# Optimization experiments

Hardware: AMD Instinct MI355X
Metric: run time of the kernel (lower is better)

## Reference

```python
import jax, jax.numpy as jnp
import numpy as np

D_MODEL = 1024
NUM_HEADS = 16
D_K = D_MODEL // NUM_HEADS


def setup_inputs() -> dict:
    key = jax.random.key(0)
    ks = jax.random.split(key, 5)
    sd = np.sqrt(2.0 / (D_MODEL + D_MODEL))
    x = jax.random.normal(ks[0], (2, 2048, D_MODEL), dtype=jnp.float32)
    # weights stored as [out_features, in_features] like torch Linear
    w_q = jax.random.normal(ks[1], (D_MODEL, D_MODEL), dtype=jnp.float32) * (sd * sd)
    w_k = jax.random.normal(ks[2], (D_MODEL, D_MODEL), dtype=jnp.float32) * (sd * sd)
    w_v = jax.random.normal(ks[3], (D_MODEL, D_MODEL), dtype=jnp.float32) * (sd * sd)
    w_o = jax.random.normal(ks[4], (D_MODEL, D_MODEL), dtype=jnp.float32) * (sd * sd)
    return {"x": x, "w_q": w_q, "w_k": w_k, "w_v": w_v, "w_o": w_o}


def reference(x, w_q, w_k, w_v, w_o):
    B, S, D = x.shape
    H, Dk = NUM_HEADS, D_K
    # projections: x @ W.T
    q = (x @ w_q.T).reshape(B, S, H, Dk).transpose(0, 2, 1, 3)  # [B,H,S,Dk]
    k = (x @ w_k.T).reshape(B, S, H, Dk).transpose(0, 2, 1, 3)
    v = (x @ w_v.T).reshape(B, S, H, Dk).transpose(0, 2, 1, 3)
    scale = 1.0 / np.sqrt(Dk).astype(np.float32)
    scores = jnp.einsum('bhqd,bhkd->bhqk', q, k) * scale  # [B,H,S,S]
    causal = jnp.tril(jnp.ones((S, S), dtype=bool))
    scores = jnp.where(causal, scores, -jnp.inf)
    weights = jax.nn.softmax(scores, axis=-1)
    attn = jnp.einsum('bhqk,bhkd->bhqd', weights, v)  # [B,H,S,Dk]
    attn = attn.transpose(0, 2, 1, 3).reshape(B, S, D)
    return attn @ w_o.T
```

## Files before the change

kernel.cpp:

```cpp
#include <hip/hip_runtime.h>

typedef __attribute__((ext_vector_type(8))) short short8;
typedef __attribute__((ext_vector_type(4))) float f32x4;
typedef __attribute__((ext_vector_type(16))) float f32x16;
typedef __attribute__((ext_vector_type(2))) unsigned int u32x2;

#define DM 1024
#define SL 2048
#define NH 16
#define DKH 64
#define NB 2

__device__ __forceinline__ unsigned short f2bf(float f) {
    union { float f; unsigned int u; } a; a.f = f;
    unsigned int r = a.u + 0x7FFFu + ((a.u >> 16) & 1u);
    return (unsigned short)(r >> 16);
}

__device__ __forceinline__ void gl_lds16(const void* g, void* l) {
    __builtin_amdgcn_global_load_lds(
        (__attribute__((address_space(1))) void*)(g),
        (__attribute__((address_space(3))) void*)(l), 16, 0, 0);
}

__device__ __forceinline__ unsigned int cvtpk_bf16(float lo, float hi) {
    unsigned int r;
    asm("v_cvt_pk_bf16_f32 %0, %1, %2" : "=v"(r) : "v"(lo), "v"(hi));
    return r;
}

__device__ __forceinline__ void pl32swap(unsigned int &a, unsigned int &b) {
    u32x2 r = __builtin_amdgcn_permlane32_swap(a, b, false, false);
    a = r[0]; b = r[1];
}
__device__ __forceinline__ void pl32swapf(float &a, float &b) {
    unsigned int ua = __float_as_uint(a), ub = __float_as_uint(b);
    pl32swap(ua, ub);
    a = __uint_as_float(ua); b = __uint_as_float(ub);
}

__global__ __launch_bounds__(256) void convert_kernel(
    const float* __restrict__ x,  const float* __restrict__ wq,
    const float* __restrict__ wk, const float* __restrict__ wv,
    const float* __restrict__ wo,
    unsigned short* __restrict__ xb,  unsigned short* __restrict__ wqb,
    unsigned short* __restrict__ wkb, unsigned short* __restrict__ wvb,
    unsigned short* __restrict__ wob)
{
    const int NX = NB * SL * DM;
    const int NW = DM * DM;
    int t4 = (blockIdx.x * 256 + threadIdx.x) * 4;
    const float* src; unsigned short* dst; int off; float scale = 1.0f;
    if (t4 < NX)              { src = x;  dst = xb;  off = t4; }
    else if (t4 < NX + NW)    { src = wq; dst = wqb; off = t4 - NX; scale = 0.125f * 1.44269504088896f; }
    else if (t4 < NX + 2*NW)  { src = wk; dst = wkb; off = t4 - NX - NW; }
    else if (t4 < NX + 3*NW)  { src = wv; dst = wvb; off = t4 - NX - 2*NW; }
    else                      { src = wo; dst = wob; off = t4 - NX - 3*NW; }
    float4 v = *(const float4*)(src + off);
    unsigned long long p =
        (unsigned long long)f2bf(v.x * scale)
      | ((unsigned long long)f2bf(v.y * scale) << 16)
      | ((unsigned long long)f2bf(v.z * scale) << 32)
      | ((unsigned long long)f2bf(v.w * scale) << 48);
    *(unsigned long long*)(dst + off) = p;
}

template<int MODE>
__global__ __launch_bounds__(256) void gemm_bt(
    const unsigned short* __restrict__ A,
    const unsigned short* __restrict__ Bw,
    unsigned short* __restrict__ oq, unsigned short* __restrict__ ok,
    unsigned short* __restrict__ ov, float* __restrict__ of)
{
    __shared__ __align__(16) unsigned short As[128 * 64];
    __shared__ __align__(16) unsigned short Bs[128 * 64];
    const int tid  = threadIdx.x;
    const int lane = tid & 63;
    const int wave = tid >> 6;
    const int wm = (wave >> 1) * 64, wn = (wave & 1) * 64;
    const int bx = blockIdx.x, by = blockIdx.y;
    const int c    = lane & 15;
    const int kg16 = (lane >> 4) * 16;
    const int swz  = (c & 7) << 4;

    f32x4 acc[4][4];
    #pragma unroll
    for (int i = 0; i < 4; i++)
        #pragma unroll
        for (int j = 0; j < 4; j++) acc[i][j] = (f32x4){0.f, 0.f, 0.f, 0.f};

    const char* Ab = (const char*)A  + by * 128 * (DM * 2);
    const char* Bb = (const char*)Bw + bx * 128 * (DM * 2);

    for (int k0 = 0; k0 < DM; k0 += 64) {
        #pragma unroll
        for (int i = 0; i < 4; i++) {
            int o  = i * 4096 + tid * 16;
            int r  = o >> 7;
            int cb = o & 127;
            int src = r * (DM * 2) + k0 * 2 + (cb ^ ((r & 7) << 4));
            gl_lds16(Ab + src, (char*)As + o);
            gl_lds16(Bb + src, (char*)Bs + o);
        }
        __syncthreads();
        #pragma unroll
        for (int kk = 0; kk < 2; kk++) {
            short8 a[4], bfr[4];
            #pragma unroll
            for (int mi = 0; mi < 4; mi++)
                a[mi] = *(const short8*)((const char*)As
                        + (wm + mi * 16 + c) * 128 + ((kk * 64 + kg16) ^ swz));
            #pragma unroll
            for (int ni = 0; ni < 4; ni++)
                bfr[ni] = *(const short8*)((const char*)Bs
                        + (wn + ni * 16 + c) * 128 + ((kk * 64 + kg16) ^ swz));
            #pragma unroll
            for (int mi = 0; mi < 4; mi++)
                #pragma unroll
                for (int ni = 0; ni < 4; ni++)
                    acc[mi][ni] = __builtin_amdgcn_mfma_f32_16x16x32_bf16(
                        a[mi], bfr[ni], acc[mi][ni], 0, 0, 0);
        }
        __syncthreads();
    }

    const int r4 = (lane >> 4) * 4;
    if (MODE == 0) {
        const int mat = (bx * 128) >> 10;
        unsigned short* outb = (mat == 0) ? oq : (mat == 1) ? ok : ov;
        const int nb = bx * 128 - (mat << 10);
        #pragma unroll
        for (int mi = 0; mi < 4; mi++) {
            int m_g = by * 128 + wm + mi * 16 + r4;
            int b_  = m_g >> 11, s_ = m_g & 2047;
            #pragma unroll
            for (int ni = 0; ni < 4; ni++) {
                int n_l = nb + wn + ni * 16 + c;
                int h = n_l >> 6, dk = n_l & 63;
                #pragma unroll
                for (int j = 0; j < 4; j++)
                    outb[((b_ * NH + h) * SL + (s_ + j)) * DKH + dk] = f2bf(acc[mi][ni][j]);
            }
        }
    } else {
        #pragma unroll
        for (int mi = 0; mi < 4; mi++) {
            int m_g = by * 128 + wm + mi * 16 + r4;
            #pragma unroll
            for (int ni = 0; ni < 4; ni++) {
                int n_g = bx * 128 + wn + ni * 16 + c;
                #pragma unroll
                for (int j = 0; j < 4; j++)
                    of[(m_g + j) * DM + n_g] = acc[mi][ni][j];
            }
        }
    }
}

__global__ __launch_bounds__(128) void attn_kernel(
    const unsigned short* __restrict__ Q,
    const unsigned short* __restrict__ K,
    const unsigned short* __restrict__ V,
    unsigned short* __restrict__ O,
    unsigned short* __restrict__ partO,
    float* __restrict__ ml)
{
    __shared__ __align__(16) unsigned short Kl[2][64 * 64];
    __shared__ __align__(16) unsigned short Vt[2][8 * 64 * 8];
    const int tid = threadIdx.x, lane = tid & 63, wave = tid >> 6;
    const int ln31 = lane & 31, hi = lane >> 5;
    const int item = blockIdx.x >> 5;
    const int bh   = blockIdx.x & 31;
    int qt, cch, t0, ntc;
    if (item < 16)      { qt = 16 + item;              cch = 0; t0 = 0;  ntc = 16; }
    else if (item < 32) { int j = item - 16; qt = 31 - j; cch = 1; t0 = 16; ntc = 16 - j; }
    else                { int j = item - 32; qt = 15 - j; cch = 0; t0 = 0;  ntc = 16 - j; }
    const int b = bh >> 4, h = bh & 15;
    const int bhi = b * NH + h;
    const unsigned short* Qg = Q + bhi * (SL * DKH);
    const unsigned short* Kg = K + bhi * (SL * DKH);
    const unsigned short* Vg = V + bhi * (SL * DKH);
    const int qw = qt * 64 + wave * 32;
    const int vd0 = (tid & 31) * 2, c0 = tid >> 5;

    short8 qf[4];
    #pragma unroll
    for (int ks = 0; ks < 4; ks++)
        qf[ks] = *(const short8*)&Qg[(qw + ln31) * DKH + ks * 16 + hi * 8];

    f32x16 OT0, OT1;
    #pragma unroll
    for (int r = 0; r < 16; r++) { OT0[r] = 0.f; OT1[r] = 0.f; }
    float mrun = -1e30f, ls = 0.f;

    unsigned int vreg[16];

    {
        const size_t kvb = (size_t)t0 * 64;
        #pragma unroll
        for (int i = 0; i < 4; i++) {
            int s = i * 128 + tid;
            int kv = s >> 3;
            int k8 = (s & 7) ^ (kv & 7);
            gl_lds16((const char*)Kg + (kvb + kv) * 128 + k8 * 16,
                     (char*)&Kl[0][0] + s * 16);
        }
        #pragma unroll
        for (int c2 = 0; c2 < 2; c2++)
            #pragma unroll
            for (int i = 0; i < 8; i++)
                vreg[c2 * 8 + i] = *(const unsigned int*)&Vg[(kvb + (c0 + 4 * c2) * 8 + i) * DKH + vd0];
    }

    for (int tt = 0; tt < ntc; ++tt) {
        const int t = t0 + tt;
        const int buf = tt & 1;
        const int kv0 = t * 64;
        #pragma unroll
        for (int c2 = 0; c2 < 2; c2++) {
            int chunk = c0 + 4 * c2;
            short8 sa, sb;
            #pragma unroll
            for (int i = 0; i < 8; i++) {
                unsigned int pr = vreg[c2 * 8 + i];
                sa[i] = (short)(pr & 0xFFFFu);
                sb[i] = (short)(pr >> 16);
            }
            *(short8*)&Vt[buf][(chunk * 64 + vd0) * 8]     = sa;
            *(short8*)&Vt[buf][(chunk * 64 + vd0 + 1) * 8] = sb;
        }
        __syncthreads();

        if (tt + 1 < ntc) {
            const size_t kv1 = (size_t)(t + 1) * 64;
            #pragma unroll
            for (int i = 0; i < 4; i++) {
                int s = i * 128 + tid;
                int kv = s >> 3;
                int k8 = (s & 7) ^ (kv & 7);
                gl_lds16((const char*)Kg + (kv1 + kv) * 128 + k8 * 16,
                         (char*)&Kl[buf ^ 1][0] + s * 16);
            }
            #pragma unroll
            for (int c2 = 0; c2 < 2; c2++)
                #pragma unroll
                for (int i = 0; i < 8; i++)
                    vreg[c2 * 8 + i] = *(const unsigned int*)&Vg[(kv1 + (c0 + 4 * c2) * 8 + i) * DKH + vd0];
        }

        const char* kb = (const char*)&Kl[buf][0];
        const unsigned short* vb = &Vt[buf][0];

        f32x16 S0, S1;
        #pragma unroll
        for (int r = 0; r < 16; r++) { S0[r] = 0.f; S1[r] = 0.f; }
        __builtin_amdgcn_s_setprio(1);
        #pragma unroll
        for (int ks = 0; ks < 4; ks++) {
            int ko = (ks * 32 + hi * 16) ^ ((ln31 & 7) << 4);
            short8 ka0 = *(const short8*)(kb + ln31 * 128 + ko);
            short8 ka1 = *(const short8*)(kb + (32 + ln31) * 128 + ko);
            S0 = __builtin_amdgcn_mfma_f32_32x32x16_bf16(ka0, qf[ks], S0, 0, 0, 0);
            S1 = __builtin_amdgcn_mfma_f32_32x32x16_bf16(ka1, qf[ks], S1, 0, 0, 0);
        }
        __builtin_amdgcn_s_setprio(0);

        if (t == qt) {
            const int qrel0 = qw + ln31 - kv0 - 4 * hi;
            const int qrel1 = qrel0 - 32;
            #pragma unroll
            for (int r = 0; r < 16; r++) {
                const int ro = (r & 3) + 8 * (r >> 2);
                if (ro > qrel0) S0[r] = -1e30f;
                if (ro > qrel1) S1[r] = -1e30f;
            }
        }

        float mx = fmaxf(S0[0], S1[0]);
        #pragma unroll
        for (int r = 1; r < 16; r++) mx = fmaxf(mx, fmaxf(S0[r], S1[r]));
        float ma = mx, mb = mx;
        pl32swapf(ma, mb);
        float rm = fmaxf(ma, mb);

        if (__any(rm > mrun + 8.f)) {
            float nm = fmaxf(mrun, rm);
            float corr = __builtin_amdgcn_exp2f(mrun - nm);
            mrun = nm; ls *= corr;
            #pragma unroll
            for (int r = 0; r < 16; r++) { OT0[r] *= corr; OT1[r] *= corr; }
        }

        float psum = 0.f;
        #pragma unroll
        for (int r = 0; r < 16; r++) {
            S0[r] = __builtin_amdgcn_exp2f(S0[r] - mrun); psum += S0[r];
            S1[r] = __builtin_amdgcn_exp2f(S1[r] - mrun); psum += S1[r];
        }
        ls += psum;

        short8 pf[4];
        {
            unsigned int wa, wb, wc, wd;
            wa = cvtpk_bf16(S0[0], S0[1]);   wb = cvtpk_bf16(S0[4], S0[5]);
            pl32swap(wa, wb);
            wc = cvtpk_bf16(S0[2], S0[3]);   wd = cvtpk_bf16(S0[6], S0[7]);
            pl32swap(wc, wd);
            union { unsigned int u[4]; short8 s; } w0 = {{wa, wc, wb, wd}};
            pf[0] = w0.s;

            wa = cvtpk_bf16(S0[8], S0[9]);   wb = cvtpk_bf16(S0[12], S0[13]);
            pl32swap(wa, wb);
            wc = cvtpk_bf16(S0[10], S0[11]); wd = cvtpk_bf16(S0[14], S0[15]);
            pl32swap(wc, wd);
            union { unsigned int u[4]; short8 s; } w1 = {{wa, wc, wb, wd}};
            pf[1] = w1.s;

            wa = cvtpk_bf16(S1[0], S1[1]);   wb = cvtpk_bf16(S1[4], S1[5]);
            pl32swap(wa, wb);
            wc = cvtpk_bf16(S1[2], S1[3]);   wd = cvtpk_bf16(S1[6], S1[7]);
            pl32swap(wc, wd);
            union { unsigned int u[4]; short8 s; } w2 = {{wa, wc, wb, wd}};
            pf[2] = w2.s;

            wa = cvtpk_bf16(S1[8], S1[9]);   wb = cvtpk_bf16(S1[12], S1[13]);
            pl32swap(wa, wb);
            wc = cvtpk_bf16(S1[10], S1[11]); wd = cvtpk_bf16(S1[14], S1[15]);
            pl32swap(wc, wd);
            union { unsigned int u[4]; short8 s; } w3 = {{wa, wc, wb, wd}};
            pf[3] = w3.s;
        }

        __builtin_amdgcn_s_setprio(1);
        #pragma unroll
        for (int ks2 = 0; ks2 < 4; ks2++) {
            int slot = (ks2 * 2 + hi) * 64;
            short8 va0 = *(const short8*)&vb[(slot + ln31) * 8];
            short8 va1 = *(const short8*)&vb[(slot + 32 + ln31) * 8];
            OT0 = __builtin_amdgcn_mfma_f32_32x32x16_bf16(va0, pf[ks2], OT0, 0, 0, 0);
            OT1 = __builtin_amdgcn_mfma_f32_32x32x16_bf16(va1, pf[ks2], OT1, 0, 0, 0);
        }
        __builtin_amdgcn_s_setprio(0);
    }

    float la = ls, lb = ls;
    pl32swapf(la, lb);
    const float lrow = la + lb;
    const int qrow_l = wave * 32 + ln31;
    if (qt >= 16) {
        const int rec = (bh * 16 + (qt - 16)) * 2 + cch;
        unsigned short* po = partO + (size_t)rec * 4096;
        if (hi == 0) {
            ml[(rec * 64 + qrow_l) * 2]     = mrun;
            ml[(rec * 64 + qrow_l) * 2 + 1] = lrow;
        }
        #pragma unroll
        for (int r = 0; r < 16; r++) {
            const int d0 = (r & 3) + 8 * (r >> 2) + 4 * hi;
            po[qrow_l * 64 + d0]      = f2bf(OT0[r]);
            po[qrow_l * 64 + 32 + d0] = f2bf(OT1[r]);
        }
    } else {
        float inv = 1.0f / lrow;
        const int qrow = qw + ln31;
        const size_t base = (size_t)(b * SL + qrow) * DM + h * DKH;
        #pragma unroll
        for (int r = 0; r < 16; r++) {
            const int d0 = (r & 3) + 8 * (r >> 2) + 4 * hi;
            O[base + d0]      = f2bf(OT0[r] * inv);
            O[base + 32 + d0] = f2bf(OT1[r] * inv);
        }
    }
}

__global__ __launch_bounds__(256) void combine_kernel(
    const unsigned short* __restrict__ partO,
    const float* __restrict__ ml,
    unsigned short* __restrict__ O)
{
    const int gi = blockIdx.x * 8 + (threadIdx.x >> 5);
    const int ln = threadIdx.x & 31;
    const int bh = gi >> 10, rem = gi & 1023;
    const int qtl = rem >> 6, row = rem & 63;
    const int qt = 16 + qtl;
    const int rec0 = (bh * 16 + qtl) * 2;
    const float m0 = ml[(rec0 * 64 + row) * 2];
    const float l0 = ml[(rec0 * 64 + row) * 2 + 1];
    const float m1 = ml[((rec0 + 1) * 64 + row) * 2];
    const float l1 = ml[((rec0 + 1) * 64 + row) * 2 + 1];
    const float M  = fmaxf(m0, m1);
    const float w0 = exp2f(m0 - M), w1 = exp2f(m1 - M);
    const float inv = 1.0f / (w0 * l0 + w1 * l1);
    const unsigned int u0 = *(const unsigned int*)&partO[(size_t)rec0 * 4096 + row * 64 + ln * 2];
    const unsigned int u1 = *(const unsigned int*)&partO[(size_t)(rec0 + 1) * 4096 + row * 64 + ln * 2];
    const float a0 = __uint_as_float(u0 << 16);
    const float b0 = __uint_as_float(u0 & 0xFFFF0000u);
    const float a1 = __uint_as_float(u1 << 16);
    const float b1 = __uint_as_float(u1 & 0xFFFF0000u);
    const float oa = (a0 * w0 + a1 * w1) * inv;
    const float ob = (b0 * w0 + b1 * w1) * inv;
    const unsigned int pack = (unsigned int)f2bf(oa) | ((unsigned int)f2bf(ob) << 16);
    const int b = bh >> 4, h = bh & 15;
    const size_t base = (size_t)(b * SL + qt * 64 + row) * DM + h * DKH;
    *(unsigned int*)&O[base + ln * 2] = pack;
}

extern "C" void kernel_launch(void* const* d_in, const int* in_sizes, int n_in,
                              void* d_out, int out_size, void* d_ws, size_t ws_size,
                              hipStream_t stream)
{
    const float* x  = (const float*)d_in[0];
    const float* wq = (const float*)d_in[1];
    const float* wk = (const float*)d_in[2];
    const float* wv = (const float*)d_in[3];
    const float* wo = (const float*)d_in[4];
    char* ws = (char*)d_ws;
    unsigned short* xb  = (unsigned short*)(ws);
    unsigned short* wqb = (unsigned short*)(ws + (8ll  << 20));
    unsigned short* wkb = (unsigned short*)(ws + (10ll << 20));
    unsigned short* wvb = (unsigned short*)(ws + (12ll << 20));
    unsigned short* wob = (unsigned short*)(ws + (14ll << 20));
    unsigned short* Qb  = (unsigned short*)(ws + (16ll << 20));
    unsigned short* Kb  = (unsigned short*)(ws + (24ll << 20));
    unsigned short* Vb  = (unsigned short*)(ws + (32ll << 20));
    unsigned short* Abf = (unsigned short*)(ws + (40ll << 20));
    unsigned short* partO = (unsigned short*)(ws);
    float*          mlbuf = (float*)(ws + (8ll << 20));
    float* out = (float*)d_out;

    convert_kernel<<<dim3(8192), dim3(256), 0, stream>>>(
        x, wq, wk, wv, wo, xb, wqb, wkb, wvb, wob);

    gemm_bt<0><<<dim3(24, 32), dim3(256), 0, stream>>>(
        xb, wqb, Qb, Kb, Vb, (float*)nullptr);

    attn_kernel<<<dim3(1536), dim3(128), 0, stream>>>(Qb, Kb, Vb, Abf, partO, mlbuf);
    combine_kernel<<<dim3(4096), dim3(256), 0, stream>>>(partO, mlbuf, Abf);

    gemm_bt<1><<<dim3(8, 32), dim3(256), 0, stream>>>(
        Abf, wob, nullptr, nullptr, nullptr, out);
}
```

Measured before the change: 111.2 us.

## Single-buffer attention LDS with register prefetch, reorder work items, split output GEMM tiles

The attention kernel drops double-buffered LDS for K and V. It prefetches the next tile into registers and writes it to a single LDS buffer after compute, which halves shared memory per block to allow more resident blocks, at the cost of an extra barrier per iteration. The order of block work items is interleaved to balance the causal workload across the launch. The output projection gets its own kernel with 64-row tiles, doubling the grid to 512 blocks so more CUs are busy, at the cost of less data reuse per tile.

```diff
diff --git a/kernel.cpp b/kernel.cpp
--- a/kernel.cpp
+++ b/kernel.cpp
@@ -65,12 +65,11 @@
     *(unsigned long long*)(dst + off) = p;
 }
 
-template<int MODE>
 __global__ __launch_bounds__(256) void gemm_bt(
     const unsigned short* __restrict__ A,
     const unsigned short* __restrict__ Bw,
     unsigned short* __restrict__ oq, unsigned short* __restrict__ ok,
-    unsigned short* __restrict__ ov, float* __restrict__ of)
+    unsigned short* __restrict__ ov)
 {
     __shared__ __align__(16) unsigned short As[128 * 64];
     __shared__ __align__(16) unsigned short Bs[128 * 64];
@@ -125,34 +124,96 @@
     }
 
     const int r4 = (lane >> 4) * 4;
-    if (MODE == 0) {
-        const int mat = (bx * 128) >> 10;
-        unsigned short* outb = (mat == 0) ? oq : (mat == 1) ? ok : ov;
-        const int nb = bx * 128 - (mat << 10);
-        #pragma unroll
-        for (int mi = 0; mi < 4; mi++) {
-            int m_g = by * 128 + wm + mi * 16 + r4;
-            int b_  = m_g >> 11, s_ = m_g & 2047;
-            #pragma unroll
-            for (int ni = 0; ni < 4; ni++) {
-                int n_l = nb + wn + ni * 16 + c;
-                int h = n_l >> 6, dk = n_l & 63;
+    const int mat = (bx * 128) >> 10;
+    unsigned short* outb = (mat == 0) ? oq : (mat == 1) ? ok : ov;
+    const int nb = bx * 128 - (mat << 10);
+    #pragma unroll
+    for (int mi = 0; mi < 4; mi++) {
+        int m_g = by * 128 + wm + mi * 16 + r4;
+        int b_  = m_g >> 11, s_ = m_g & 2047;
+        #pragma unroll
+        for (int ni = 0; ni < 4; ni++) {
+            int n_l = nb + wn + ni * 16 + c;
+            int h = n_l >> 6, dk = n_l & 63;
+            #pragma unroll
+            for (int j = 0; j < 4; j++)
+                outb[((b_ * NH + h) * SL + (s_ + j)) * DKH + dk] = f2bf(acc[mi][ni][j]);
+        }
+    }
+}
+
+__global__ __launch_bounds__(256) void gemm_o(
+    const unsigned short* __restrict__ A,
+    const unsigned short* __restrict__ Bw,
+    float* __restrict__ of)
+{
+    __shared__ __align__(16) unsigned short As[64 * 64];
+    __shared__ __align__(16) unsigned short Bs[128 * 64];
+    const int tid  = threadIdx.x;
+    const int lane = tid & 63;
+    const int wave = tid >> 6;
+    const int wm = (wave >> 1) * 32, wn = (wave & 1) * 64;
+    const int bx = blockIdx.x, by = blockIdx.y;
+    const int c    = lane & 15;
+    const int kg16 = (lane >> 4) * 16;
+    const int swz  = (c & 7) << 4;
+
+    f32x4 acc[2][4];
+    #pragma unroll
+    for (int i = 0; i < 2; i++)
+        #pragma unroll
+        for (int j = 0; j < 4; j++) acc[i][j] = (f32x4){0.f, 0.f, 0.f, 0.f};
+
+    const char* Ab = (const char*)A  + by * 64  * (DM * 2);
+    const char* Bb = (const char*)Bw + bx * 128 * (DM * 2);
+
+    for (int k0 = 0; k0 < DM; k0 += 64) {
+        #pragma unroll
+        for (int i = 0; i < 2; i++) {
+            int o  = i * 4096 + tid * 16;
+            int r  = o >> 7, cb = o & 127;
+            int src = r * (DM * 2) + k0 * 2 + (cb ^ ((r & 7) << 4));
+            gl_lds16(Ab + src, (char*)As + o);
+        }
+        #pragma unroll
+        for (int i = 0; i < 4; i++) {
+            int o  = i * 4096 + tid * 16;
+            int r  = o >> 7, cb = o & 127;
+            int src = r * (DM * 2) + k0 * 2 + (cb ^ ((r & 7) << 4));
+            gl_lds16(Bb + src, (char*)Bs + o);
+        }
+        __syncthreads();
+        #pragma unroll
+        for (int kk = 0; kk < 2; kk++) {
+            short8 a[2], bfr[4];
+            #pragma unroll
+            for (int mi = 0; mi < 2; mi++)
+                a[mi] = *(const short8*)((const char*)As
+                        + (wm + mi * 16 + c) * 128 + ((kk * 64 + kg16) ^ swz));
+            #pragma unroll
+            for (int ni = 0; ni < 4; ni++)
+                bfr[ni] = *(const short8*)((const char*)Bs
+                        + (wn + ni * 16 + c) * 128 + ((kk * 64 + kg16) ^ swz));
+            #pragma unroll
+            for (int mi = 0; mi < 2; mi++)
                 #pragma unroll
-                for (int j = 0; j < 4; j++)
-                    outb[((b_ * NH + h) * SL + (s_ + j)) * DKH + dk] = f2bf(acc[mi][ni][j]);
-            }
-        }
-    } else {
-        #pragma unroll
-        for (int mi = 0; mi < 4; mi++) {
-            int m_g = by * 128 + wm + mi * 16 + r4;
-            #pragma unroll
-            for (int ni = 0; ni < 4; ni++) {
-                int n_g = bx * 128 + wn + ni * 16 + c;
-                #pragma unroll
-                for (int j = 0; j < 4; j++)
-                    of[(m_g + j) * DM + n_g] = acc[mi][ni][j];
-            }
+                for (int ni = 0; ni < 4; ni++)
+                    acc[mi][ni] = __builtin_amdgcn_mfma_f32_16x16x32_bf16(
+                        a[mi], bfr[ni], acc[mi][ni], 0, 0, 0);
+        }
+        __syncthreads();
+    }
+
+    const int r4 = (lane >> 4) * 4;
+    #pragma unroll
+    for (int mi = 0; mi < 2; mi++) {
+        int m_g = by * 64 + wm + mi * 16 + r4;
+        #pragma unroll
+        for (int ni = 0; ni < 4; ni++) {
+            int n_g = bx * 128 + wn + ni * 16 + c;
+            #pragma unroll
+            for (int j = 0; j < 4; j++)
+                of[(m_g + j) * DM + n_g] = acc[mi][ni][j];
         }
     }
 }
@@ -165,12 +226,19 @@
     unsigned short* __restrict__ partO,
     float* __restrict__ ml)
 {
-    __shared__ __align__(16) unsigned short Kl[2][64 * 64];
-    __shared__ __align__(16) unsigned short Vt[2][8 * 64 * 8];
+    __shared__ __align__(16) unsigned short Kl[64 * 64];
+    __shared__ __align__(16) unsigned short Vt[8 * 64 * 8];
     const int tid = threadIdx.x, lane = tid & 63, wave = tid >> 6;
     const int ln31 = lane & 31, hi = lane >> 5;
-    const int item = blockIdx.x >> 5;
-    const int bh   = blockIdx.x & 31;
+    const int m  = blockIdx.x >> 5;
+    const int bh = blockIdx.x & 31;
+    const int rr = m >> 3, g = m & 7;
+    int item;
+    if (rr < 2)       item = m;
+    else if (rr == 2) item = 16 + g;
+    else if (rr == 3) item = 31 - g;
+    else if (rr == 4) item = 32 + g;
+    else              item = 47 - g;
     int qt, cch, t0, ntc;
     if (item < 16)      { qt = 16 + item;              cch = 0; t0 = 0;  ntc = 16; }
     else if (item < 32) { int j = item - 16; qt = 31 - j; cch = 1; t0 = 16; ntc = 16 - j; }
@@ -193,29 +261,29 @@
     for (int r = 0; r < 16; r++) { OT0[r] = 0.f; OT1[r] = 0.f; }
     float mrun = -1e30f, ls = 0.f;
 
+    short8 kreg[4];
     unsigned int vreg[16];
+
 
     {
         const size_t kvb = (size_t)t0 * 64;
         #pragma unroll
         for (int i = 0; i < 4; i++) {
             int s = i * 128 + tid;
-            int kv = s >> 3;
-            int k8 = (s & 7) ^ (kv & 7);
-            gl_lds16((const char*)Kg + (kvb + kv) * 128 + k8 * 16,
-                     (char*)&Kl[0][0] + s * 16);
+            int kv = s >> 3, k8 = s & 7;
+            kreg[i] = *(const short8*)&Kg[(kvb + kv) * DKH + k8 * 8];
         }
         #pragma unroll
         for (int c2 = 0; c2 < 2; c2++)
             #pragma unroll
             for (int i = 0; i < 8; i++)
                 vreg[c2 * 8 + i] = *(const unsigned int*)&Vg[(kvb + (c0 + 4 * c2) * 8 + i) * DKH + vd0];
-    }
-
-    for (int tt = 0; tt < ntc; ++tt) {
-        const int t = t0 + tt;
-        const int buf = tt & 1;
-        const int kv0 = t * 64;
+        #pragma unroll
+        for (int i = 0; i < 4; i++) {
+            int s = i * 128 + tid;
+            int kv = s >> 3, k8 = (s & 7) ^ (kv & 7);
+            *(short8*)((char*)Kl + kv * 128 + k8 * 16) = kreg[i];
+        }
         #pragma unroll
         for (int c2 = 0; c2 < 2; c2++) {
             int chunk = c0 + 4 * c2;
@@ -226,20 +294,23 @@
                 sa[i] = (short)(pr & 0xFFFFu);
                 sb[i] = (short)(pr >> 16);
             }
-            *(short8*)&Vt[buf][(chunk * 64 + vd0) * 8]     = sa;
-            *(short8*)&Vt[buf][(chunk * 64 + vd0 + 1) * 8] = sb;
+            *(short8*)&Vt[(chunk * 64 + vd0) * 8]     = sa;
+            *(short8*)&Vt[(chunk * 64 + vd0 + 1) * 8] = sb;
         }
         __syncthreads();
+    }
+
+    for (int tt = 0; tt < ntc; ++tt) {
+        const int t = t0 + tt;
+        const int kv0 = t * 64;
 
         if (tt + 1 < ntc) {
             const size_t kv1 = (size_t)(t + 1) * 64;
             #pragma unroll
             for (int i = 0; i < 4; i++) {
                 int s = i * 128 + tid;
-                int kv = s >> 3;
-                int k8 = (s & 7) ^ (kv & 7);
-                gl_lds16((const char*)Kg + (kv1 + kv) * 128 + k8 * 16,
-                         (char*)&Kl[buf ^ 1][0] + s * 16);
+                int kv = s >> 3, k8 = s & 7;
+                kreg[i] = *(const short8*)&Kg[(kv1 + kv) * DKH + k8 * 8];
             }
             #pragma unroll
             for (int c2 = 0; c2 < 2; c2++)
@@ -248,9 +319,6 @@
                     vreg[c2 * 8 + i] = *(const unsigned int*)&Vg[(kv1 + (c0 + 4 * c2) * 8 + i) * DKH + vd0];
         }
 
-        const char* kb = (const char*)&Kl[buf][0];
-        const unsigned short* vb = &Vt[buf][0];
-
         f32x16 S0, S1;
         #pragma unroll
         for (int r = 0; r < 16; r++) { S0[r] = 0.f; S1[r] = 0.f; }
@@ -258,8 +326,8 @@
         #pragma unroll
         for (int ks = 0; ks < 4; ks++) {
             int ko = (ks * 32 + hi * 16) ^ ((ln31 & 7) << 4);
-            short8 ka0 = *(const short8*)(kb + ln31 * 128 + ko);
-            short8 ka1 = *(const short8*)(kb + (32 + ln31) * 128 + ko);
+            short8 ka0 = *(const short8*)((const char*)Kl + ln31 * 128 + ko);
+            short8 ka1 = *(const short8*)((const char*)Kl + (32 + ln31) * 128 + ko);
             S0 = __builtin_amdgcn_mfma_f32_32x32x16_bf16(ka0, qf[ks], S0, 0, 0, 0);
             S1 = __builtin_amdgcn_mfma_f32_32x32x16_bf16(ka1, qf[ks], S1, 0, 0, 0);
         }
@@ -335,12 +403,36 @@
         #pragma unroll
         for (int ks2 = 0; ks2 < 4; ks2++) {
             int slot = (ks2 * 2 + hi) * 64;
-            short8 va0 = *(const short8*)&vb[(slot + ln31) * 8];
-            short8 va1 = *(const short8*)&vb[(slot + 32 + ln31) * 8];
+            short8 va0 = *(const short8*)&Vt[(slot + ln31) * 8];
+            short8 va1 = *(const short8*)&Vt[(slot + 32 + ln31) * 8];
             OT0 = __builtin_amdgcn_mfma_f32_32x32x16_bf16(va0, pf[ks2], OT0, 0, 0, 0);
             OT1 = __builtin_amdgcn_mfma_f32_32x32x16_bf16(va1, pf[ks2], OT1, 0, 0, 0);
         }
         __builtin_amdgcn_s_setprio(0);
+
+        if (tt + 1 < ntc) {
+            __syncthreads();
+            #pragma unroll
+            for (int i = 0; i < 4; i++) {
+                int s = i * 128 + tid;
+                int kv = s >> 3, k8 = (s & 7) ^ (kv & 7);
+                *(short8*)((char*)Kl + kv * 128 + k8 * 16) = kreg[i];
+            }
+            #pragma unroll
+            for (int c2 = 0; c2 < 2; c2++) {
+                int chunk = c0 + 4 * c2;
+                short8 sa, sb;
+                #pragma unroll
+                for (int i = 0; i < 8; i++) {
+                    unsigned int pr = vreg[c2 * 8 + i];
+                    sa[i] = (short)(pr & 0xFFFFu);
+                    sb[i] = (short)(pr >> 16);
+                }
+                *(short8*)&Vt[(chunk * 64 + vd0) * 8]     = sa;
+                *(short8*)&Vt[(chunk * 64 + vd0 + 1) * 8] = sb;
+            }
+            __syncthreads();
+        }
     }
 
     float la = ls, lb = ls;
@@ -431,12 +523,10 @@
     convert_kernel<<<dim3(8192), dim3(256), 0, stream>>>(
         x, wq, wk, wv, wo, xb, wqb, wkb, wvb, wob);
 
-    gemm_bt<0><<<dim3(24, 32), dim3(256), 0, stream>>>(
-        xb, wqb, Qb, Kb, Vb, (float*)nullptr);
+    gemm_bt<<<dim3(24, 32), dim3(256), 0, stream>>>(xb, wqb, Qb, Kb, Vb);
 
     attn_kernel<<<dim3(1536), dim3(128), 0, stream>>>(Qb, Kb, Vb, Abf, partO, mlbuf);
     combine_kernel<<<dim3(4096), dim3(256), 0, stream>>>(partO, mlbuf, Abf);
 
-    gemm_bt<1><<<dim3(8, 32), dim3(256), 0, stream>>>(
-        Abf, wob, nullptr, nullptr, nullptr, out);
-}
+    gemm_o<<<dim3(8, 64), dim3(256), 0, stream>>>(Abf, wob, out);
+}
```

New measurement: 110.3 us. No clear change (-0.9%).
